# Kernel tuning notes

Hardware: AMD Instinct MI355X
Metric: run time of the kernel (lower is better)

Reference implementation:

```python
import jax, jax.numpy as jnp
import numpy as np

ENT_TYPES = 9
INNER_DIM = 64


def setup_inputs() -> dict:
    key = jax.random.key(0)
    k1, k2 = jax.random.split(key)
    B, S, H = 8, 1024, 768
    last_hidden_state = jax.random.normal(k1, (B, S, H), dtype=jnp.float32)
    attention_mask = jnp.ones((B, S), dtype=jnp.float32)
    dense_w = jax.random.normal(k2, (ENT_TYPES * INNER_DIM * 2, H), dtype=jnp.float32) * (1.0 / np.sqrt(H))
    dense_b = jnp.zeros((ENT_TYPES * INNER_DIM * 2,), dtype=jnp.float32)
    return {
        "last_hidden_state": last_hidden_state,
        "attention_mask": attention_mask,
        "dense_w": dense_w,
        "dense_b": dense_b,
    }


def _sinusoidal_pos_emb(seq_len: int, output_dim: int, dtype):
    # (seq_len, output_dim) interleaved as [sin0, cos0, sin1, cos1, ...]
    position = jnp.arange(seq_len, dtype=dtype)[:, None]              # (S, 1)
    indices = jnp.arange(output_dim // 2, dtype=dtype)
    inv_freq = jnp.power(jnp.asarray(10000.0, dtype), -2.0 * indices / output_dim)
    ang = position * inv_freq                                         # (S, D/2)
    emb = jnp.stack([jnp.sin(ang), jnp.cos(ang)], axis=-1)            # (S, D/2, 2)
    return emb.reshape(seq_len, output_dim)


def reference(last_hidden_state, attention_mask, dense_w, dense_b):
    B, S, H = last_hidden_state.shape
    D = INNER_DIM
    E = ENT_TYPES

    # dense projection then split into per-entity-type q/k of width D each
    out = last_hidden_state @ dense_w.T + dense_b                     # (B, S, 2*E*D)
    out = out.reshape(B, S, E, 2 * D)                                 # (B, S, E, 2D)
    qw, kw = out[..., :D], out[..., D:]                               # (B, S, E, D)

    # RoPE: duplicated cos/sin pairs, half-rotation
    pos = _sinusoidal_pos_emb(S, D, last_hidden_state.dtype)          # (S, D)
    cos_pos = jnp.repeat(pos[:, 1::2], 2, axis=-1)[None, :, None, :]  # (1, S, 1, D)
    sin_pos = jnp.repeat(pos[:, 0::2], 2, axis=-1)[None, :, None, :]

    def rotate_half(x):
        x1, x2 = x[..., : D // 2], x[..., D // 2 :]
        return jnp.concatenate([-x2, x1], axis=-1)

    qw = qw * cos_pos + rotate_half(qw) * sin_pos
    kw = kw * cos_pos + rotate_half(kw) * sin_pos

    # pairwise entity scores
    logits = jnp.einsum("bmhd,bnhd->bhmn", qw, kw) / jnp.sqrt(jnp.asarray(D, logits_dtype := last_hidden_state.dtype))

    # padding mask along key axis (as in original)
    pad_mask = attention_mask[:, None, None, :]                       # (B, 1, 1, S)
    logits = logits * pad_mask - (1.0 - pad_mask) * 10000.0

    # upper-triangular validity mask (start <= end)
    tri = jnp.triu(jnp.ones((S, S), dtype=logits.dtype))[None, None]  # (1, 1, S, S)
    logits = logits - (1.0 - tri) * 10000.0
    return logits
```

## Files before the change

kernel.cpp:

```cpp
#include <hip/hip_runtime.h>

#define BB 8
#define SS 1024
#define HH 768
#define EE 9
#define DD 64
#define NCOL (EE * 2 * DD)

typedef __bf16 bf16x8 __attribute__((ext_vector_type(8)));
typedef float f32x4 __attribute__((ext_vector_type(4)));

__device__ __forceinline__ unsigned short f2b(float f) {
    unsigned int x = __float_as_uint(f);
    unsigned int r = (x + 0x7fffu + ((x >> 16) & 1u)) >> 16;
    return (unsigned short)r;
}

__device__ __forceinline__ void gload_lds16(const void* g, void* l) {
    __builtin_amdgcn_global_load_lds(
        (const __attribute__((address_space(1))) void*)g,
        (__attribute__((address_space(3))) void*)l, 16, 0, 0);
}

__global__ __launch_bounds__(256) void to_bf16_2(
    const float* __restrict__ a, int n4a,
    const float* __restrict__ w, int n4w,
    unsigned short* __restrict__ oa,
    unsigned short* __restrict__ ow) {
    int i = blockIdx.x * 256 + threadIdx.x;
    const float* src;
    unsigned short* dst;
    int j;
    if (i < n4a) {
        src = a; dst = oa; j = i;
    } else {
        j = i - n4a;
        if (j >= n4w) return;
        src = w; dst = ow;
    }
    float4 v = ((const float4*)src)[j];
    ushort4 o = {f2b(v.x), f2b(v.y), f2b(v.z), f2b(v.w)};
    ((ushort4*)dst)[j] = o;
}

__global__ __launch_bounds__(256) void dense_rope_mfma(
    const unsigned short* __restrict__ Abf,
    const unsigned short* __restrict__ Wbf,
    const float* __restrict__ bias,
    unsigned short* __restrict__ q_ws,
    unsigned short* __restrict__ k_ws) {
    __shared__ unsigned short As[128 * 32];
    __shared__ unsigned short Bs[128 * 32];

    const int t = threadIdx.x;
    const int lane = t & 63, wave = t >> 6;
    const int quad = lane >> 4, lr = lane & 15;
    const int wm = wave >> 1, wn = wave & 1;
    const int j0 = blockIdx.x * 128;
    const int m0 = blockIdx.y * 128;

    f32x4 acc[4][4] = {};

    const int srow = wave * 16 + (lane >> 2);
    const int sc8 = (lane & 3) * 8;

    for (int kt = 0; kt < HH / 32; ++kt) {
        const int k0 = kt * 32;
        __syncthreads();
#pragma unroll
        for (int i = 0; i < 2; ++i) {
            const int row = i * 64 + srow;
            const int lb = i * 2048 + wave * 512;
            gload_lds16(&Abf[(size_t)(m0 + row) * HH + k0 + sc8], &As[lb]);
            gload_lds16(&Wbf[(size_t)(j0 + row) * HH + k0 + sc8], &Bs[lb]);
        }
        __syncthreads();

        bf16x8 af[4], bf[4];
#pragma unroll
        for (int nt = 0; nt < 4; ++nt)
            af[nt] = *(const bf16x8*)&Bs[(wn * 64 + nt * 16 + lr) * 32 + quad * 8];
#pragma unroll
        for (int st = 0; st < 4; ++st)
            bf[st] = *(const bf16x8*)&As[(wm * 64 + st * 16 + lr) * 32 + quad * 8];
#pragma unroll
        for (int nt = 0; nt < 4; ++nt)
#pragma unroll
            for (int st = 0; st < 4; ++st)
                acc[nt][st] = __builtin_amdgcn_mfma_f32_16x16x32_bf16(
                    af[nt], bf[st], acc[nt][st], 0, 0, 0);
    }

    const int gcol0 = j0 + wn * 64;
    const int g = gcol0 >> 6;
    const int e = g >> 1;
    unsigned short* dst = (g & 1) ? k_ws : q_ws;
    const int b_idx = m0 >> 10;
    const size_t zbase = (size_t)(b_idx * EE + e) * SS;
    const float L2C = 0.4152410118609203f;

    float4 bb[4];
    float iv0[4], iv1[4];
#pragma unroll
    for (int nt = 0; nt < 4; ++nt) {
        bb[nt] = *(const float4*)&bias[gcol0 + nt * 16 + quad * 4];
        const int h0 = nt * 8 + quad * 2;
        iv0[nt] = exp2f(-(float)h0 * L2C);
        iv1[nt] = exp2f(-(float)(h0 + 1) * L2C);
    }
    const int s0 = (m0 & (SS - 1)) + wm * 64;
#pragma unroll
    for (int st = 0; st < 4; ++st) {
        const int s = s0 + st * 16 + lr;
        const float sf = (float)s;
        float c[4][4];
#pragma unroll
        for (int nt = 0; nt < 4; ++nt) {
            c[nt][0] = acc[nt][st][0] + bb[nt].x;
            c[nt][1] = acc[nt][st][1] + bb[nt].y;
            c[nt][2] = acc[nt][st][2] + bb[nt].z;
            c[nt][3] = acc[nt][st][3] + bb[nt].w;
        }
        unsigned short* drow = &dst[(zbase + s) * DD + quad * 4];
#pragma unroll
        for (int nt = 0; nt < 4; ++nt) {
            float sv0, cv0, sv1, cv1;
            __sincosf(sf * iv0[nt], &sv0, &cv0);
            __sincosf(sf * iv1[nt], &sv1, &cv1);
            float r0 = (nt < 2) ? -c[nt + 2][0] : c[nt - 2][0];
            float r1 = (nt < 2) ? -c[nt + 2][1] : c[nt - 2][1];
            float r2 = (nt < 2) ? -c[nt + 2][2] : c[nt - 2][2];
            float r3 = (nt < 2) ? -c[nt + 2][3] : c[nt - 2][3];
            ushort4 o = {f2b(c[nt][0] * cv0 + r0 * sv0),
                         f2b(c[nt][1] * cv0 + r1 * sv0),
                         f2b(c[nt][2] * cv1 + r2 * sv1),
                         f2b(c[nt][3] * cv1 + r3 * sv1)};
            *(ushort4*)&drow[nt * 16] = o;
        }
    }
}

__global__ __launch_bounds__(256) void logits_mfma(
    const unsigned short* __restrict__ q_ws,
    const unsigned short* __restrict__ k_ws,
    const float* __restrict__ mask,
    float* __restrict__ out) {
    const int t = threadIdx.x;
    const int lane = t & 63, wave = t >> 6;
    const int quad = lane >> 4, lr = lane & 15;
    const int wm = wave >> 1, wn = wave & 1;
    const int n0 = blockIdx.x * 128;
    const int m0 = blockIdx.y * 128;
    const int z = blockIdx.z;
    const int b_idx = z / EE;

    const unsigned short* kb =
        k_ws + ((size_t)z * SS + n0 + wn * 64 + lr) * DD + quad * 8;
    const unsigned short* qb =
        q_ws + ((size_t)z * SS + m0 + wm * 64 + lr) * DD + quad * 8;

    bf16x8 af[2][4], bf[2][4];
#pragma unroll
    for (int x = 0; x < 4; ++x) {
        af[0][x] = *(const bf16x8*)&kb[(size_t)(x * 16) * DD];
        af[1][x] = *(const bf16x8*)&kb[(size_t)(x * 16) * DD + 32];
        bf[0][x] = *(const bf16x8*)&qb[(size_t)(x * 16) * DD];
        bf[1][x] = *(const bf16x8*)&qb[(size_t)(x * 16) * DD + 32];
    }

    f32x4 acc[4][4] = {};
#pragma unroll
    for (int ks = 0; ks < 2; ++ks)
#pragma unroll
        for (int nt = 0; nt < 4; ++nt)
#pragma unroll
            for (int mt = 0; mt < 4; ++mt)
                acc[nt][mt] = __builtin_amdgcn_mfma_f32_16x16x32_bf16(
                    af[ks][nt], bf[ks][mt], acc[nt][mt], 0, 0, 0);

    const int nb0 = n0 + wn * 64;
    float4 pv[4];
#pragma unroll
    for (int nt = 0; nt < 4; ++nt)
        pv[nt] = *(const float4*)&mask[b_idx * SS + nb0 + nt * 16 + quad * 4];

    float* outz = out + (size_t)z * SS * SS;
#pragma unroll
    for (int mt = 0; mt < 4; ++mt) {
        const int m = m0 + wm * 64 + mt * 16 + lr;
        float* rowp = &outz[(size_t)m * SS];
#pragma unroll
        for (int nt = 0; nt < 4; ++nt) {
            const int nb = nb0 + nt * 16 + quad * 4;
            f32x4 v;
#pragma unroll
            for (int reg = 0; reg < 4; ++reg) {
                const float p = (&pv[nt].x)[reg];
                float x = acc[nt][mt][reg] * 0.125f;
                x = x * p - (1.0f - p) * 10000.0f;
                if (nb + reg < m) x -= 10000.0f;
                v[reg] = x;
            }
            *(f32x4*)(rowp + nb) = v;
        }
    }
}

extern "C" void kernel_launch(void* const* d_in, const int* in_sizes, int n_in,
                              void* d_out, int out_size, void* d_ws, size_t ws_size,
                              hipStream_t stream) {
    const float* lhs  = (const float*)d_in[0];
    const float* mask = (const float*)d_in[1];
    const float* W    = (const float*)d_in[2];
    const float* bias = (const float*)d_in[3];
    float* out = (float*)d_out;

    unsigned short* q_ws = (unsigned short*)d_ws;
    unsigned short* k_ws = q_ws + (size_t)BB * EE * SS * DD;
    unsigned short* Abf  = k_ws + (size_t)BB * EE * SS * DD;
    unsigned short* Wbf  = Abf + (size_t)BB * SS * HH;

    const int n4a = (BB * SS * HH) / 4;
    const int n4w = (NCOL * HH) / 4;
    const int nconv = (n4a + n4w + 255) / 256;
    to_bf16_2<<<nconv, 256, 0, stream>>>(lhs, n4a, W, n4w, Abf, Wbf);

    dim3 g1(NCOL / 128, (BB * SS) / 128);
    dense_rope_mfma<<<g1, 256, 0, stream>>>(Abf, Wbf, bias, q_ws, k_ws);

    dim3 g2(SS / 128, SS / 128, BB * EE);
    logits_mfma<<<g2, 256, 0, stream>>>(q_ws, k_ws, mask, out);
}
```

Baseline: 383.0 us.

## Stage Q/K tiles through padded LDS and swap MFMA operand roles for scalar stores

The logits kernel now loads Q and K tiles cooperatively with coalesced 16-byte global reads into padded LDS, then reads MFMA fragments from shared memory instead of doing strided per-lane global loads. It also swaps the MFMA operand order so that each lane holds consecutive rows rather than consecutive columns. As a result the output is written as scalar floats in which 16 lanes cover 16 adjacent columns, replacing the per-lane float4 stores. The intent is cheaper input loading, but it trades vector 16-byte stores for 4-byte stores on the dominant 300MB output write, which may hurt write efficiency.

```diff
diff --git a/kernel.cpp b/kernel.cpp
--- a/kernel.cpp
+++ b/kernel.cpp
@@ -140,11 +140,15 @@
     }
 }
 
+#define LDA2 72
 __global__ __launch_bounds__(256) void logits_mfma(
     const unsigned short* __restrict__ q_ws,
     const unsigned short* __restrict__ k_ws,
     const float* __restrict__ mask,
     float* __restrict__ out) {
+    __shared__ unsigned short Qs[128 * LDA2];
+    __shared__ unsigned short Ks[128 * LDA2];
+
     const int t = threadIdx.x;
     const int lane = t & 63, wave = t >> 6;
     const int quad = lane >> 4, lr = lane & 15;
@@ -154,54 +158,56 @@
     const int z = blockIdx.z;
     const int b_idx = z / EE;
 
-    const unsigned short* kb =
-        k_ws + ((size_t)z * SS + n0 + wn * 64 + lr) * DD + quad * 8;
-    const unsigned short* qb =
-        q_ws + ((size_t)z * SS + m0 + wm * 64 + lr) * DD + quad * 8;
-
-    bf16x8 af[2][4], bf[2][4];
-#pragma unroll
-    for (int x = 0; x < 4; ++x) {
-        af[0][x] = *(const bf16x8*)&kb[(size_t)(x * 16) * DD];
-        af[1][x] = *(const bf16x8*)&kb[(size_t)(x * 16) * DD + 32];
-        bf[0][x] = *(const bf16x8*)&qb[(size_t)(x * 16) * DD];
-        bf[1][x] = *(const bf16x8*)&qb[(size_t)(x * 16) * DD + 32];
-    }
+    const uint4* qsrc = (const uint4*)(q_ws + ((size_t)z * SS + m0) * DD);
+    const uint4* ksrc = (const uint4*)(k_ws + ((size_t)z * SS + n0) * DD);
+#pragma unroll
+    for (int i = 0; i < 4; ++i) {
+        int idx = t + i * 256;
+        int row = idx >> 3, c8 = (idx & 7) * 8;
+        uint4 qv = qsrc[idx];
+        uint4 kv = ksrc[idx];
+        *(uint4*)&Qs[row * LDA2 + c8] = qv;
+        *(uint4*)&Ks[row * LDA2 + c8] = kv;
+    }
+    __syncthreads();
 
     f32x4 acc[4][4] = {};
 #pragma unroll
-    for (int ks = 0; ks < 2; ++ks)
+    for (int ks = 0; ks < DD; ks += 32) {
+        bf16x8 af[4], bf[4];
+#pragma unroll
+        for (int mt = 0; mt < 4; ++mt)
+            af[mt] = *(const bf16x8*)&Qs[(wm * 64 + mt * 16 + lr) * LDA2 + ks + quad * 8];
 #pragma unroll
         for (int nt = 0; nt < 4; ++nt)
-#pragma unroll
-            for (int mt = 0; mt < 4; ++mt)
-                acc[nt][mt] = __builtin_amdgcn_mfma_f32_16x16x32_bf16(
-                    af[ks][nt], bf[ks][mt], acc[nt][mt], 0, 0, 0);
-
-    const int nb0 = n0 + wn * 64;
-    float4 pv[4];
+            bf[nt] = *(const bf16x8*)&Ks[(wn * 64 + nt * 16 + lr) * LDA2 + ks + quad * 8];
+#pragma unroll
+        for (int mt = 0; mt < 4; ++mt)
+#pragma unroll
+            for (int nt = 0; nt < 4; ++nt)
+                acc[mt][nt] = __builtin_amdgcn_mfma_f32_16x16x32_bf16(
+                    af[mt], bf[nt], acc[mt][nt], 0, 0, 0);
+    }
+
+    float p[4];
 #pragma unroll
     for (int nt = 0; nt < 4; ++nt)
-        pv[nt] = *(const float4*)&mask[b_idx * SS + nb0 + nt * 16 + quad * 4];
+        p[nt] = mask[b_idx * SS + n0 + wn * 64 + nt * 16 + lr];
 
     float* outz = out + (size_t)z * SS * SS;
 #pragma unroll
     for (int mt = 0; mt < 4; ++mt) {
-        const int m = m0 + wm * 64 + mt * 16 + lr;
-        float* rowp = &outz[(size_t)m * SS];
-#pragma unroll
-        for (int nt = 0; nt < 4; ++nt) {
-            const int nb = nb0 + nt * 16 + quad * 4;
-            f32x4 v;
-#pragma unroll
-            for (int reg = 0; reg < 4; ++reg) {
-                const float p = (&pv[nt].x)[reg];
-                float x = acc[nt][mt][reg] * 0.125f;
-                x = x * p - (1.0f - p) * 10000.0f;
-                if (nb + reg < m) x -= 10000.0f;
-                v[reg] = x;
+#pragma unroll
+        for (int reg = 0; reg < 4; ++reg) {
+            const int m = m0 + wm * 64 + mt * 16 + quad * 4 + reg;
+#pragma unroll
+            for (int nt = 0; nt < 4; ++nt) {
+                const int n = n0 + wn * 64 + nt * 16 + lr;
+                float v = acc[mt][nt][reg] * 0.125f;
+                v = v * p[nt] - (1.0f - p[nt]) * 10000.0f;
+                if (n < m) v -= 10000.0f;
+                outz[(size_t)m * SS + n] = v;
             }
-            *(f32x4*)(rowp + nb) = v;
         }
     }
 }
```

Result: faster. 368.5 us (-3.8%).
